# Kernel tuning notes

Hardware: AMD Instinct MI355X
Metric: run time of the kernel (lower is better)

Reference implementation:

```python
import jax, jax.numpy as jnp
import numpy as np
from jax import lax

FEATURE_DIM = 1024
KERNEL_SIZE = 4
PAD = KERNEL_SIZE - 1  # causal left padding


def setup_inputs() -> dict:
    key = jax.random.key(0)
    k_x, k_w = jax.random.split(key)
    B, T, F = 8, 8192, FEATURE_DIM
    x = jax.random.normal(k_x, (B, T, F), dtype=jnp.float32)
    # depthwise kernel, flax 'WIO' layout with feature_group_count=F: (K, in/groups=1, F)
    # lecun_normal over fan_in = kernel_size * in_per_group = 4
    fan_in = KERNEL_SIZE * 1
    W = jax.random.normal(k_w, (KERNEL_SIZE, 1, F), dtype=jnp.float32) * (1.0 / np.sqrt(fan_in))
    b = jnp.zeros((F,), dtype=jnp.float32)
    return {"x": x, "W": W, "b": b}


def reference(x, W, b):
    # Original pads (PAD, PAD) symmetrically then slices off the trailing PAD steps;
    # mathematically identical to left-only padding of PAD, which avoids the
    # wasted tail computation while producing the exact same values.
    y = lax.conv_general_dilated(
        x, W,
        window_strides=(1,),
        padding=[(PAD, 0)],
        dimension_numbers=("NWC", "WIO", "NWC"),
        feature_group_count=FEATURE_DIM,
    )
    return y + b  # (B, T, F)
```

## Files before the change

### kernel.cpp

```cpp
#include <hip/hip_runtime.h>


constexpr int FEAT   = 1024;
constexpr int F4     = FEAT / 4;
constexpr int TSTEPS = 8192;
constexpr int TT     = 16;
constexpr int NTILE  = TSTEPS / TT;

__global__ __launch_bounds__(256) void causal_conv1d_kernel(
    const float4* __restrict__ x4,
    const float*  __restrict__ W,
    const float*  __restrict__ bias,
    float4*       __restrict__ y4)
{
    int idx = blockIdx.x * blockDim.x + threadIdx.x;
    int f4    = idx & (F4 - 1);
    int tmp   = idx >> 8;
    int ttile = tmp & (NTILE - 1);
    int batch = tmp >> 9;

    int t0 = ttile * TT;
    int base = (batch * TSTEPS + t0) * F4 + f4;

    const float4* W4 = reinterpret_cast<const float4*>(W);
    float4 w0 = W4[0 * F4 + f4];
    float4 w1 = W4[1 * F4 + f4];
    float4 w2 = W4[2 * F4 + f4];
    float4 w3 = W4[3 * F4 + f4];
    float4 bb = reinterpret_cast<const float4*>(bias)[f4];

    float4 h0 = {0.f, 0.f, 0.f, 0.f};
    float4 h1 = h0, h2 = h0;
    if (t0 > 0) {
        h0 = x4[base - 3 * F4];
        h1 = x4[base - 2 * F4];
        h2 = x4[base - 1 * F4];
    }

#pragma unroll
    for (int i = 0; i < TT; ++i) {
        float4 cur = x4[base + i * F4];
        float4 o;
        o.x = fmaf(w3.x, cur.x, fmaf(w2.x, h2.x, fmaf(w1.x, h1.x, fmaf(w0.x, h0.x, bb.x))));
        o.y = fmaf(w3.y, cur.y, fmaf(w2.y, h2.y, fmaf(w1.y, h1.y, fmaf(w0.y, h0.y, bb.y))));
        o.z = fmaf(w3.z, cur.z, fmaf(w2.z, h2.z, fmaf(w1.z, h1.z, fmaf(w0.z, h0.z, bb.z))));
        o.w = fmaf(w3.w, cur.w, fmaf(w2.w, h2.w, fmaf(w1.w, h1.w, fmaf(w0.w, h0.w, bb.w))));
        y4[base + i * F4] = o;
        h0 = h1; h1 = h2; h2 = cur;
    }
}

extern "C" void kernel_launch(void* const* d_in, const int* in_sizes, int n_in,
                              void* d_out, int out_size, void* d_ws, size_t ws_size,
                              hipStream_t stream) {
    const float4* x4 = (const float4*)d_in[0];
    const float*  W  = (const float*)d_in[1];
    const float*  b  = (const float*)d_in[2];
    float4* y4 = (float4*)d_out;

    constexpr int B = 8;
    int total_threads = B * NTILE * F4;
    int block = 256;
    int grid  = total_threads / block;
    causal_conv1d_kernel<<<grid, block, 0, stream>>>(x4, W, b, y4);
}
```

Before: 101.6 us.

## Batch loads per chunk, add nontemporal stores, XCD-aware block remap, larger time tile

```diff
diff --git a/kernel.cpp b/kernel.cpp
--- a/kernel.cpp
+++ b/kernel.cpp
@@ -1,62 +1,78 @@
 #include <hip/hip_runtime.h>
 
+
+typedef float f32x4 __attribute__((ext_vector_type(4)));
 
 constexpr int FEAT   = 1024;
 constexpr int F4     = FEAT / 4;
 constexpr int TSTEPS = 8192;
-constexpr int TT     = 16;
+constexpr int TT     = 32;
 constexpr int NTILE  = TSTEPS / TT;
+constexpr int NXCD   = 8;
 
 __global__ __launch_bounds__(256) void causal_conv1d_kernel(
-    const float4* __restrict__ x4,
-    const float*  __restrict__ W,
-    const float*  __restrict__ bias,
-    float4*       __restrict__ y4)
+    const f32x4* __restrict__ x4,
+    const float* __restrict__ W,
+    const float* __restrict__ bias,
+    f32x4*       __restrict__ y4)
 {
-    int idx = blockIdx.x * blockDim.x + threadIdx.x;
+    int nblk = gridDim.x;
+    int bid  = blockIdx.x;
+    int lid  = (bid % NXCD) * (nblk / NXCD) + bid / NXCD;
+
+    int idx = lid * 256 + threadIdx.x;
     int f4    = idx & (F4 - 1);
     int tmp   = idx >> 8;
     int ttile = tmp & (NTILE - 1);
-    int batch = tmp >> 9;
+    int batch = tmp >> 8;
 
     int t0 = ttile * TT;
     int base = (batch * TSTEPS + t0) * F4 + f4;
 
-    const float4* W4 = reinterpret_cast<const float4*>(W);
-    float4 w0 = W4[0 * F4 + f4];
-    float4 w1 = W4[1 * F4 + f4];
-    float4 w2 = W4[2 * F4 + f4];
-    float4 w3 = W4[3 * F4 + f4];
-    float4 bb = reinterpret_cast<const float4*>(bias)[f4];
+    const f32x4* W4 = reinterpret_cast<const f32x4*>(W);
+    f32x4 w0 = W4[0 * F4 + f4];
+    f32x4 w1 = W4[1 * F4 + f4];
+    f32x4 w2 = W4[2 * F4 + f4];
+    f32x4 w3 = W4[3 * F4 + f4];
+    f32x4 bb = reinterpret_cast<const f32x4*>(bias)[f4];
 
-    float4 h0 = {0.f, 0.f, 0.f, 0.f};
-    float4 h1 = h0, h2 = h0;
+    f32x4 h0 = {0.f, 0.f, 0.f, 0.f};
+    f32x4 h1 = h0, h2 = h0;
     if (t0 > 0) {
         h0 = x4[base - 3 * F4];
         h1 = x4[base - 2 * F4];
         h2 = x4[base - 1 * F4];
     }
 
+    for (int c = 0; c < TT / 8; ++c) {
+        f32x4 cur[8];
 #pragma unroll
-    for (int i = 0; i < TT; ++i) {
-        float4 cur = x4[base + i * F4];
-        float4 o;
-        o.x = fmaf(w3.x, cur.x, fmaf(w2.x, h2.x, fmaf(w1.x, h1.x, fmaf(w0.x, h0.x, bb.x))));
-        o.y = fmaf(w3.y, cur.y, fmaf(w2.y, h2.y, fmaf(w1.y, h1.y, fmaf(w0.y, h0.y, bb.y))));
-        o.z = fmaf(w3.z, cur.z, fmaf(w2.z, h2.z, fmaf(w1.z, h1.z, fmaf(w0.z, h0.z, bb.z))));
-        o.w = fmaf(w3.w, cur.w, fmaf(w2.w, h2.w, fmaf(w1.w, h1.w, fmaf(w0.w, h0.w, bb.w))));
-        y4[base + i * F4] = o;
-        h0 = h1; h1 = h2; h2 = cur;
+        for (int i = 0; i < 8; ++i)
+            cur[i] = x4[base + (c * 8 + i) * F4];
+#pragma unroll
+        for (int i = 0; i < 8; ++i) {
+            f32x4 p0 = (i >= 3) ? cur[i - 3] : (i == 0 ? h0 : (i == 1 ? h1 : h2));
+            f32x4 p1 = (i >= 2) ? cur[i - 2] : (i == 0 ? h1 : h2);
+            f32x4 p2 = (i >= 1) ? cur[i - 1] : h2;
+            f32x4 p3 = cur[i];
+            f32x4 o;
+            o.x = fmaf(w3.x, p3.x, fmaf(w2.x, p2.x, fmaf(w1.x, p1.x, fmaf(w0.x, p0.x, bb.x))));
+            o.y = fmaf(w3.y, p3.y, fmaf(w2.y, p2.y, fmaf(w1.y, p1.y, fmaf(w0.y, p0.y, bb.y))));
+            o.z = fmaf(w3.z, p3.z, fmaf(w2.z, p2.z, fmaf(w1.z, p1.z, fmaf(w0.z, p0.z, bb.z))));
+            o.w = fmaf(w3.w, p3.w, fmaf(w2.w, p2.w, fmaf(w1.w, p1.w, fmaf(w0.w, p0.w, bb.w))));
+            __builtin_nontemporal_store(o, &y4[base + (c * 8 + i) * F4]);
+        }
+        h0 = cur[5]; h1 = cur[6]; h2 = cur[7];
     }
 }
 
 extern "C" void kernel_launch(void* const* d_in, const int* in_sizes, int n_in,
                               void* d_out, int out_size, void* d_ws, size_t ws_size,
                               hipStream_t stream) {
-    const float4* x4 = (const float4*)d_in[0];
-    const float*  W  = (const float*)d_in[1];
-    const float*  b  = (const float*)d_in[2];
-    float4* y4 = (float4*)d_out;
+    const f32x4* x4 = (const f32x4*)d_in[0];
+    const float* W  = (const float*)d_in[1];
+    const float* b  = (const float*)d_in[2];
+    f32x4* y4 = (f32x4*)d_out;
 
     constexpr int B = 8;
     int total_threads = B * NTILE * F4;
```

Measured after the change: 86.32 us. -15.0%, faster.
